# Kernel tuning notes

Hardware: AMD Instinct MI355X
Metric: run time of the kernel (lower is better)

Reference implementation:

```python
import jax, jax.numpy as jnp
import numpy as np

N_NODES = 50000
N_EDGES = 800000
D_IN = 64
D_OUT = 64


def setup_inputs() -> dict:
    key = jax.random.key(0)
    k1, k2, k3 = jax.random.split(key, 3)
    features = jax.random.normal(k1, (N_NODES, D_IN), dtype=jnp.float32)
    W = jax.random.normal(k2, (D_IN, D_OUT), dtype=jnp.float32) * (1.0 / np.sqrt(D_IN))
    b = jnp.zeros((D_OUT,), dtype=jnp.float32)
    edge_index = jax.random.randint(k3, (2, N_EDGES), 0, N_NODES, dtype=jnp.int64)
    return {"features": features, "W": W, "b": b, "edge_index": edge_index}


def reference(features, W, b, edge_index):
    # PyG GCNConv: add self-loops, symmetric normalization D^{-1/2}(A+I)D^{-1/2},
    # then aggregate x[row] at col (source -> target), plus linear + bias.
    N = features.shape[0]
    loop = jnp.arange(N, dtype=edge_index.dtype)
    row = jnp.concatenate([edge_index[0], loop])  # source nodes
    col = jnp.concatenate([edge_index[1], loop])  # target nodes

    ones = jnp.ones(row.shape[0], dtype=features.dtype)
    deg = jax.ops.segment_sum(ones, col, num_segments=N)  # in-degree incl. self-loop
    dinv = jnp.where(deg > 0, jax.lax.rsqrt(deg), 0.0)
    norm = dinv[row] * dinv[col]  # [E+N]

    x = features @ W                          # [N, D_OUT], tiny GEMM
    msg = x[row] * norm[:, None]              # gather + scale  [E+N, D_OUT]
    out = jax.ops.segment_sum(msg, col, num_segments=N)  # scatter-add
    return out + b
```

## Files before the change

### kernel.cpp

```cpp
#include <hip/hip_runtime.h>
#include <hip/hip_fp16.h>

#define NN 50000
#define NE 800000
#define D  64
#define NBUK 256
#define CHUNK (NE / NBUK)
#define FS 68

typedef float __attribute__((ext_vector_type(4))) f32x4;

__device__ inline int block_exscan(int val, int tid) {
    __shared__ int wsum[4];
    int lane = tid & 63, w = tid >> 6;
    int v = val;
    #pragma unroll
    for (int d = 1; d < 64; d <<= 1) {
        int t = __shfl_up(v, d);
        if (lane >= d) v += t;
    }
    if (lane == 63) wsum[w] = v;
    __syncthreads();
    int base = 0;
    #pragma unroll
    for (int i = 0; i < 4; ++i) base += (i < w) ? wsum[i] : 0;
    __syncthreads();
    return base + v - val;
}

__global__ __launch_bounds__(256) void k_hist(const int* __restrict__ col,
                                              int* __restrict__ H) {
    __shared__ int h[NBUK];
    const int tid = threadIdx.x, blk = blockIdx.x;
    h[tid] = 0;
    __syncthreads();
    const int base = blk * CHUNK;
    for (int i = tid; i < CHUNK; i += 256)
        atomicAdd(&h[col[base + i] >> 8], 1);
    __syncthreads();
    H[tid * NBUK + blk] = h[tid];
}

__global__ __launch_bounds__(256) void k_scanA(int* __restrict__ H,
                                               int* __restrict__ bsum) {
    const int tid = threadIdx.x, blk = blockIdx.x;
    const int i = blk * 256 + tid;
    int val = H[i];
    int ex = block_exscan(val, tid);
    H[i] = ex;
    if (tid == 255) bsum[blk] = ex + val;
}

__global__ __launch_bounds__(256) void k_bucket(const int* __restrict__ row,
                                                const int* __restrict__ col,
                                                const int* __restrict__ H,
                                                const int* __restrict__ bsum,
                                                unsigned int* __restrict__ packed) {
    __shared__ int base_l[NBUK];
    __shared__ int rank[NBUK];
    const int tid = threadIdx.x, blk = blockIdx.x;
    int ex = block_exscan(bsum[tid], tid);
    base_l[tid] = ex + H[tid * NBUK + blk];
    rank[tid] = 0;
    __syncthreads();
    const int base = blk * CHUNK;
    for (int i = tid; i < CHUNK; i += 256) {
        int c = col[base + i], r = row[base + i];
        int bk = c >> 8;
        int rk = atomicAdd(&rank[bk], 1);
        packed[base_l[bk] + rk] =
            (unsigned)(r & 0xFFFF) | ((unsigned)(c & 0xFF) << 16);
    }
}

__global__ __launch_bounds__(256) void k_csr(const unsigned int* __restrict__ packed,
                                             const int* __restrict__ bsum,
                                             int* __restrict__ off,
                                             int* __restrict__ cnt,
                                             unsigned short* __restrict__ csr) {
    __shared__ int exs[NBUK];
    __shared__ int ncnt[NBUK];
    __shared__ int nbase[NBUK];
    __shared__ int rk2[NBUK];
    const int tid = threadIdx.x, b = blockIdx.x;
    int ex = block_exscan(bsum[tid], tid);
    exs[tid] = ex;
    ncnt[tid] = 0;
    rk2[tid] = 0;
    __syncthreads();
    const int start = exs[b];
    const int size  = bsum[b];
    for (int i = tid; i < size; i += 256)
        atomicAdd(&ncnt[(packed[start + i] >> 16) & 0xFF], 1);
    __syncthreads();
    int v2  = ncnt[tid];
    int ex2 = block_exscan(v2, tid);
    const int node = b * NBUK + tid;
    off[node] = start + ex2;
    cnt[node] = v2;
    nbase[tid] = start + ex2;
    __syncthreads();
    for (int i = tid; i < size; i += 256) {
        unsigned u = packed[start + i];
        int ln = (u >> 16) & 0xFF;
        int rk = atomicAdd(&rk2[ln], 1);
        csr[nbase[ln] + rk] = (unsigned short)(u & 0xFFFF);
    }
}

__global__ __launch_bounds__(256) void k_gemm(const float* __restrict__ feat,
                                              const float* __restrict__ W,
                                              const int* __restrict__ cnt,
                                              __half* __restrict__ y) {
    __shared__ float feat_lds[64 * FS];
    __shared__ float W_lds[D * D];

    const int tid   = threadIdx.x;
    const int rbase = blockIdx.x * 64;

    {
        const float4* W4  = reinterpret_cast<const float4*>(W);
        float4*       Wl4 = reinterpret_cast<float4*>(W_lds);
        for (int i = tid; i < D * D / 4; i += 256) Wl4[i] = W4[i];
    }
    {
        const int k0 = (tid & 15) * 4;
        #pragma unroll
        for (int it = 0; it < 4; ++it) {
            int r  = it * 16 + (tid >> 4);
            int gr = rbase + r;
            float4 v = make_float4(0.f, 0.f, 0.f, 0.f);
            if (gr < NN) v = *reinterpret_cast<const float4*>(&feat[gr * D + k0]);
            *reinterpret_cast<float4*>(&feat_lds[r * FS + k0]) = v;
        }
    }
    __syncthreads();

    const int tx = tid & 15;
    const int ty = tid >> 4;

    float acc[4][4] = {};

    #pragma unroll 8
    for (int k = 0; k < D; ++k) {
        float4 w = *reinterpret_cast<const float4*>(&W_lds[k * D + tx * 4]);
        float f0 = feat_lds[(ty * 4 + 0) * FS + k];
        float f1 = feat_lds[(ty * 4 + 1) * FS + k];
        float f2 = feat_lds[(ty * 4 + 2) * FS + k];
        float f3 = feat_lds[(ty * 4 + 3) * FS + k];
        acc[0][0] = fmaf(f0, w.x, acc[0][0]); acc[0][1] = fmaf(f0, w.y, acc[0][1]);
        acc[0][2] = fmaf(f0, w.z, acc[0][2]); acc[0][3] = fmaf(f0, w.w, acc[0][3]);
        acc[1][0] = fmaf(f1, w.x, acc[1][0]); acc[1][1] = fmaf(f1, w.y, acc[1][1]);
        acc[1][2] = fmaf(f1, w.z, acc[1][2]); acc[1][3] = fmaf(f1, w.w, acc[1][3]);
        acc[2][0] = fmaf(f2, w.x, acc[2][0]); acc[2][1] = fmaf(f2, w.y, acc[2][1]);
        acc[2][2] = fmaf(f2, w.z, acc[2][2]); acc[2][3] = fmaf(f2, w.w, acc[2][3]);
        acc[3][0] = fmaf(f3, w.x, acc[3][0]); acc[3][1] = fmaf(f3, w.y, acc[3][1]);
        acc[3][2] = fmaf(f3, w.z, acc[3][2]); acc[3][3] = fmaf(f3, w.w, acc[3][3]);
    }

    #pragma unroll
    for (int i = 0; i < 4; ++i) {
        int gr = rbase + ty * 4 + i;
        if (gr < NN) {
            float s = rsqrtf((float)cnt[gr] + 1.0f);
            __half2 h0 = __floats2half2_rn(acc[i][0] * s, acc[i][1] * s);
            __half2 h1 = __floats2half2_rn(acc[i][2] * s, acc[i][3] * s);
            union { __half2 h[2]; uint2 u; } p;
            p.h[0] = h0; p.h[1] = h1;
            *reinterpret_cast<uint2*>(&y[gr * D + tx * 4]) = p.u;
        }
    }
}

__global__ __launch_bounds__(256) void k_agg8(const unsigned short* __restrict__ csr,
                                              const int* __restrict__ off,
                                              const int* __restrict__ cnt,
                                              const __half* __restrict__ y,
                                              const float* __restrict__ b,
                                              float* __restrict__ out) {
    const int lane = threadIdx.x & 63;
    const int g    = lane >> 3;
    const int l8   = lane & 7;
    const int wave = blockIdx.x * 4 + (threadIdx.x >> 6);
    const int c    = wave * 8 + g;
    const bool valid = (c < NN);

    const uint4* y16 = reinterpret_cast<const uint4*>(y);

    const int s = valid ? off[c] : 0;
    const int n = valid ? cnt[c] : 0;

    int maxn = n;
    maxn = max(maxn, __shfl_xor(maxn, 8));
    maxn = max(maxn, __shfl_xor(maxn, 16));
    maxn = max(maxn, __shfl_xor(maxn, 32));

    int pre0 = (l8      < n) ? (int)csr[s + l8     ] : 0;
    int pre1 = (l8 + 8  < n) ? (int)csr[s + l8 + 8 ] : 0;
    int pre2 = (l8 + 16 < n) ? (int)csr[s + l8 + 16] : 0;
    int pre3 = (l8 + 24 < n) ? (int)csr[s + l8 + 24] : 0;

    float acc[8] = {0.f, 0.f, 0.f, 0.f, 0.f, 0.f, 0.f, 0.f};

    auto addm = [&](uint4 u, float m) {
        const __half2* h = reinterpret_cast<const __half2*>(&u);
        float2 f0 = __half22float2(h[0]);
        float2 f1 = __half22float2(h[1]);
        float2 f2 = __half22float2(h[2]);
        float2 f3 = __half22float2(h[3]);
        acc[0] = fmaf(m, f0.x, acc[0]); acc[1] = fmaf(m, f0.y, acc[1]);
        acc[2] = fmaf(m, f1.x, acc[2]); acc[3] = fmaf(m, f1.y, acc[3]);
        acc[4] = fmaf(m, f2.x, acc[4]); acc[5] = fmaf(m, f2.y, acc[5]);
        acc[6] = fmaf(m, f3.x, acc[6]); acc[7] = fmaf(m, f3.y, acc[7]);
    };

    {
        int cs = valid ? c : 0;
        uint4 u = y16[cs * 8 + l8];
        addm(u, valid ? 1.0f : 0.0f);
    }

    const int srcb = lane & 56;

    #pragma unroll
    for (int w = 0; w < 4; ++w) {
        if (w * 8 < maxn) {
            const int pw = (w == 0) ? pre0 : (w == 1) ? pre1
                         : (w == 2) ? pre2 : pre3;
            uint4 u[8];
            float msk[8];
            #pragma unroll
            for (int e = 0; e < 8; ++e) {
                int r = __shfl(pw, srcb + e);
                u[e] = y16[r * 8 + l8];
                msk[e] = (w * 8 + e < n) ? 1.0f : 0.0f;
            }
            #pragma unroll
            for (int e = 0; e < 8; ++e) addm(u[e], msk[e]);
        }
    }

    for (int i = 32; i < n; ++i) {
        int r = (int)csr[s + i];
        addm(y16[r * 8 + l8], 1.0f);
    }

    if (valid) {
        float sc = rsqrtf((float)n + 1.0f);
        const float4* b4 = reinterpret_cast<const float4*>(b);
        float4 bb0 = b4[l8 * 2], bb1 = b4[l8 * 2 + 1];
        f32x4 o0, o1;
        o0.x = acc[0] * sc + bb0.x;  o0.y = acc[1] * sc + bb0.y;
        o0.z = acc[2] * sc + bb0.z;  o0.w = acc[3] * sc + bb0.w;
        o1.x = acc[4] * sc + bb1.x;  o1.y = acc[5] * sc + bb1.y;
        o1.z = acc[6] * sc + bb1.z;  o1.w = acc[7] * sc + bb1.w;
        f32x4* out4 = reinterpret_cast<f32x4*>(out);
        __builtin_nontemporal_store(o0, &out4[c * 16 + l8 * 2]);
        __builtin_nontemporal_store(o1, &out4[c * 16 + l8 * 2 + 1]);
    }
}

extern "C" void kernel_launch(void* const* d_in, const int* in_sizes, int n_in,
                              void* d_out, int out_size, void* d_ws, size_t ws_size,
                              hipStream_t stream) {
    const float* feat = (const float*)d_in[0];
    const float* W    = (const float*)d_in[1];
    const float* b    = (const float*)d_in[2];
    const int*   ei   = (const int*)d_in[3];
    const int*   row  = ei;
    const int*   col  = ei + NE;

    float* out = (float*)d_out;

    int*            H      = (int*)d_ws;
    int*            bsum   = H + 65536;
    int*            cnt    = bsum + 1024;
    int*            off    = cnt + 65536;
    unsigned int*   packed = (unsigned int*)(off + 65536);
    unsigned short* csr    = (unsigned short*)(packed + NE);
    __half*         y      = (__half*)(csr + NE);

    k_hist  <<<NBUK, 256, 0, stream>>>(col, H);
    k_scanA <<<NBUK, 256, 0, stream>>>(H, bsum);
    k_bucket<<<NBUK, 256, 0, stream>>>(row, col, H, bsum, packed);
    k_csr   <<<NBUK, 256, 0, stream>>>(packed, bsum, off, cnt, csr);
    k_gemm  <<<(NN + 63) / 64, 256, 0, stream>>>(feat, W, cnt, y);
    k_agg8  <<<(NN + 31) / 32, 256, 0, stream>>>(csr, off, cnt, y, b, out);
}
```

Baseline: 57.70 us.

## Split fp16 projected features into two feature halves for aggregation

The GEMM output is stored as two separate 32-column fp16 arrays, and the aggregation kernel runs two blocks per node group, each gathering only one half. Each half-array is 3.2 MB, so the randomly gathered working set per block is smaller and more likely to stay cache-resident. In exchange the CSR indices, offsets and counts are read twice, and each gather is 64 bytes instead of 128. Nontemporal loads are also used for the index metadata.

```diff
diff --git a/kernel.cpp b/kernel.cpp
--- a/kernel.cpp
+++ b/kernel.cpp
@@ -111,7 +111,8 @@
 __global__ __launch_bounds__(256) void k_gemm(const float* __restrict__ feat,
                                               const float* __restrict__ W,
                                               const int* __restrict__ cnt,
-                                              __half* __restrict__ y) {
+                                              __half* __restrict__ y0,
+                                              __half* __restrict__ y1) {
     __shared__ float feat_lds[64 * FS];
     __shared__ float W_lds[D * D];
 
@@ -158,6 +159,7 @@
         acc[3][2] = fmaf(f3, w.z, acc[3][2]); acc[3][3] = fmaf(f3, w.w, acc[3][3]);
     }
 
+    const int d0 = tx * 4;
     #pragma unroll
     for (int i = 0; i < 4; ++i) {
         int gr = rbase + ty * 4 + i;
@@ -167,38 +169,42 @@
             __half2 h1 = __floats2half2_rn(acc[i][2] * s, acc[i][3] * s);
             union { __half2 h[2]; uint2 u; } p;
             p.h[0] = h0; p.h[1] = h1;
-            *reinterpret_cast<uint2*>(&y[gr * D + tx * 4]) = p.u;
+            __half* dst = (d0 < 32) ? &y0[gr * 32 + d0] : &y1[gr * 32 + (d0 - 32)];
+            *reinterpret_cast<uint2*>(dst) = p.u;
         }
     }
 }
 
-__global__ __launch_bounds__(256) void k_agg8(const unsigned short* __restrict__ csr,
+__global__ __launch_bounds__(256) void k_agg4(const unsigned short* __restrict__ csr,
                                               const int* __restrict__ off,
                                               const int* __restrict__ cnt,
-                                              const __half* __restrict__ y,
+                                              const __half* __restrict__ y0,
+                                              const __half* __restrict__ y1,
                                               const float* __restrict__ b,
                                               float* __restrict__ out) {
     const int lane = threadIdx.x & 63;
-    const int g    = lane >> 3;
-    const int l8   = lane & 7;
-    const int wave = blockIdx.x * 4 + (threadIdx.x >> 6);
-    const int c    = wave * 8 + g;
+    const int g    = lane >> 2;
+    const int l4   = lane & 3;
+    const int half = blockIdx.x & 1;
+    const int wave = (blockIdx.x >> 1) * 4 + (threadIdx.x >> 6);
+    const int c    = wave * 16 + g;
     const bool valid = (c < NN);
 
-    const uint4* y16 = reinterpret_cast<const uint4*>(y);
-
-    const int s = valid ? off[c] : 0;
-    const int n = valid ? cnt[c] : 0;
+    const __half* yh = half ? y1 : y0;
+    const uint4* y16 = reinterpret_cast<const uint4*>(yh);
+
+    const int s = valid ? __builtin_nontemporal_load(&off[c]) : 0;
+    const int n = valid ? __builtin_nontemporal_load(&cnt[c]) : 0;
 
     int maxn = n;
-    maxn = max(maxn, __shfl_xor(maxn, 8));
-    maxn = max(maxn, __shfl_xor(maxn, 16));
-    maxn = max(maxn, __shfl_xor(maxn, 32));
-
-    int pre0 = (l8      < n) ? (int)csr[s + l8     ] : 0;
-    int pre1 = (l8 + 8  < n) ? (int)csr[s + l8 + 8 ] : 0;
-    int pre2 = (l8 + 16 < n) ? (int)csr[s + l8 + 16] : 0;
-    int pre3 = (l8 + 24 < n) ? (int)csr[s + l8 + 24] : 0;
+    #pragma unroll
+    for (int m = 4; m <= 32; m <<= 1) maxn = max(maxn, __shfl_xor(maxn, m));
+
+    int pre[8];
+    #pragma unroll
+    for (int k = 0; k < 8; ++k)
+        pre[k] = (l4 + 4 * k < n)
+               ? (int)__builtin_nontemporal_load(&csr[s + l4 + 4 * k]) : 0;
 
     float acc[8] = {0.f, 0.f, 0.f, 0.f, 0.f, 0.f, 0.f, 0.f};
 
@@ -216,24 +222,22 @@
 
     {
         int cs = valid ? c : 0;
-        uint4 u = y16[cs * 8 + l8];
-        addm(u, valid ? 1.0f : 0.0f);
-    }
-
-    const int srcb = lane & 56;
+        addm(y16[cs * 4 + l4], valid ? 1.0f : 0.0f);
+    }
+
+    const int srcb = lane & 60;
 
     #pragma unroll
     for (int w = 0; w < 4; ++w) {
         if (w * 8 < maxn) {
-            const int pw = (w == 0) ? pre0 : (w == 1) ? pre1
-                         : (w == 2) ? pre2 : pre3;
             uint4 u[8];
             float msk[8];
             #pragma unroll
             for (int e = 0; e < 8; ++e) {
-                int r = __shfl(pw, srcb + e);
-                u[e] = y16[r * 8 + l8];
-                msk[e] = (w * 8 + e < n) ? 1.0f : 0.0f;
+                const int idx = w * 8 + e;
+                int r = __shfl(pre[idx >> 2], srcb + (idx & 3));
+                u[e] = y16[r * 4 + l4];
+                msk[e] = (idx < n) ? 1.0f : 0.0f;
             }
             #pragma unroll
             for (int e = 0; e < 8; ++e) addm(u[e], msk[e]);
@@ -242,21 +246,21 @@
 
     for (int i = 32; i < n; ++i) {
         int r = (int)csr[s + i];
-        addm(y16[r * 8 + l8], 1.0f);
+        addm(y16[r * 4 + l4], 1.0f);
     }
 
     if (valid) {
         float sc = rsqrtf((float)n + 1.0f);
         const float4* b4 = reinterpret_cast<const float4*>(b);
-        float4 bb0 = b4[l8 * 2], bb1 = b4[l8 * 2 + 1];
+        float4 bb0 = b4[half * 8 + l4 * 2], bb1 = b4[half * 8 + l4 * 2 + 1];
         f32x4 o0, o1;
         o0.x = acc[0] * sc + bb0.x;  o0.y = acc[1] * sc + bb0.y;
         o0.z = acc[2] * sc + bb0.z;  o0.w = acc[3] * sc + bb0.w;
         o1.x = acc[4] * sc + bb1.x;  o1.y = acc[5] * sc + bb1.y;
         o1.z = acc[6] * sc + bb1.z;  o1.w = acc[7] * sc + bb1.w;
         f32x4* out4 = reinterpret_cast<f32x4*>(out);
-        __builtin_nontemporal_store(o0, &out4[c * 16 + l8 * 2]);
-        __builtin_nontemporal_store(o1, &out4[c * 16 + l8 * 2 + 1]);
+        __builtin_nontemporal_store(o0, &out4[c * 16 + half * 8 + l4 * 2]);
+        __builtin_nontemporal_store(o1, &out4[c * 16 + half * 8 + l4 * 2 + 1]);
     }
 }
 
@@ -278,12 +282,13 @@
     int*            off    = cnt + 65536;
     unsigned int*   packed = (unsigned int*)(off + 65536);
     unsigned short* csr    = (unsigned short*)(packed + NE);
-    __half*         y      = (__half*)(csr + NE);
+    __half*         y0     = (__half*)(csr + NE);
+    __half*         y1     = y0 + NN * 32;
 
     k_hist  <<<NBUK, 256, 0, stream>>>(col, H);
     k_scanA <<<NBUK, 256, 0, stream>>>(H, bsum);
     k_bucket<<<NBUK, 256, 0, stream>>>(row, col, H, bsum, packed);
     k_csr   <<<NBUK, 256, 0, stream>>>(packed, bsum, off, cnt, csr);
-    k_gemm  <<<(NN + 63) / 64, 256, 0, stream>>>(feat, W, cnt, y);
-    k_agg8  <<<(NN + 31) / 32, 256, 0, stream>>>(csr, off, cnt, y, b, out);
-}
+    k_gemm  <<<(NN + 63) / 64, 256, 0, stream>>>(feat, W, cnt, y0, y1);
+    k_agg4  <<<2 * ((NN + 63) / 64), 256, 0, stream>>>(csr, off, cnt, y0, y1, b, out);
+}
```

Result: slower. 62.00 us (+7.4%).
